# Kernel optimization log

Hardware: AMD Instinct MI355X
Metric: run time of the kernel (lower is better)

## Reference

```python
import jax, jax.numpy as jnp
import numpy as np


def setup_inputs() -> dict:
    key = jax.random.key(0)
    ks = jax.random.split(key, 4)
    B, C, H, W = 8, 256, 64, 64
    C8 = C // 8
    x = jax.random.normal(ks[0], (B, C, H, W), dtype=jnp.float32)
    wq = jax.random.normal(ks[1], (C8, C), dtype=jnp.float32) * 0.05
    wk = jax.random.normal(ks[2], (C8, C), dtype=jnp.float32) * 0.05
    wv = jax.random.normal(ks[3], (C, C), dtype=jnp.float32) * 0.05
    bq = jnp.zeros((C8,), jnp.float32)
    bk = jnp.zeros((C8,), jnp.float32)
    bv = jnp.zeros((C,), jnp.float32)
    return {"x": x, "wq": wq, "bq": bq, "wk": wk, "bk": bk, "wv": wv, "bv": bv}


def _conv1x1(x, w, b):
    # x: [B,C,H,W], w: [O,C], b: [O] -> [B,O,H,W]
    return jnp.einsum('bchw,oc->bohw', x, w) + b[None, :, None, None]


def reference(x, wq, bq, wk, bk, wv, bv):
    B, C, H, W = x.shape
    N = H * W
    q = _conv1x1(x, wq, bq).reshape(B, -1, N)   # [B, C/8, N]
    k = _conv1x1(x, wk, bk).reshape(B, -1, N)   # [B, C/8, N]
    v = _conv1x1(x, wv, bv).reshape(B, C, N)    # [B, C, N]
    # energy[b, n, m] = sum_c q[b, c, n] * k[b, c, m]
    energy = jnp.einsum('bcn,bcm->bnm', q, k)   # [B, N, N]
    attn = jax.nn.softmax(energy, axis=-1)
    # out[b, c, n] = sum_m v[b, c, m] * attn[b, n, m]
    out = jnp.einsum('bcm,bnm->bcn', v, attn)   # [B, C, N]
    return out.reshape(B, C, H, W) + x
```

## Files before the change

### kernel.cpp

```cpp
#include <hip/hip_runtime.h>

#define B_ 8
#define C_ 256
#define C8_ 32
#define N_ 4096

typedef __bf16 bf16;
typedef __bf16 bf16x4 __attribute__((ext_vector_type(4)));
typedef __bf16 bf16x8 __attribute__((ext_vector_type(8)));
typedef float f32x4 __attribute__((ext_vector_type(4)));
typedef float f32x16 __attribute__((ext_vector_type(16)));

#if __has_builtin(__builtin_amdgcn_exp2f)
#define EXP2 __builtin_amdgcn_exp2f
#else
#define EXP2 exp2f
#endif

#define CVTPK(lo, hi) ({ unsigned int _w;                                     \
  asm("v_cvt_pk_bf16_f32 %0, %1, %2" : "=v"(_w) : "v"(lo), "v"(hi)); _w; })
#define LSWAP(a, b) asm("v_permlane32_swap_b32 %0, %1" : "+v"(a), "+v"(b))

#define GLD16(gp, lp) __builtin_amdgcn_global_load_lds(                       \
    (const __attribute__((address_space(1))) void*)(gp),                      \
    (__attribute__((address_space(3))) void*)(lp), 16, 0, 0)
#define VMW(n) do { asm volatile("s_waitcnt vmcnt(" n ")" ::: "memory");      \
    __builtin_amdgcn_sched_barrier(0); } while (0)
#define RBAR() __builtin_amdgcn_s_barrier()

__global__ __launch_bounds__(256) void k_convw(const float* __restrict__ wq,
    const float* __restrict__ wk, const float* __restrict__ wv,
    bf16* __restrict__ Wb) {
  int i = (blockIdx.x * 256 + threadIdx.x) * 4;
  const float* src; int off;
  if (i < 8192) { src = wq; off = i; }
  else if (i < 16384) { src = wk; off = i - 8192; }
  else { src = wv; off = i - 16384; }
  f32x4 v = *reinterpret_cast<const f32x4*>(src + off);
  bf16x4 o;
  o[0] = (bf16)v[0]; o[1] = (bf16)v[1]; o[2] = (bf16)v[2]; o[3] = (bf16)v[3];
  *reinterpret_cast<bf16x4*>(Wb + i) = o;
}

__global__ __launch_bounds__(256) void k_transpose(const float* __restrict__ x,
                                                   bf16* __restrict__ xT) {
  __shared__ bf16 t[64][72];
  int bid = blockIdx.x;
  int b = bid & 7, rem = bid >> 3;
  int c0 = (rem >> 6) * 64, n0 = (rem & 63) * 64;
  int tid = threadIdx.x;
#pragma unroll
  for (int r = 0; r < 4; ++r) {
    int cc = r * 16 + (tid >> 4);
    int j = (tid & 15) * 4;
    f32x4 v = *reinterpret_cast<const f32x4*>(
        x + ((size_t)b * C_ + c0 + cc) * N_ + n0 + j);
    bf16x4 o;
    o[0] = (bf16)v[0]; o[1] = (bf16)v[1]; o[2] = (bf16)v[2]; o[3] = (bf16)v[3];
    *reinterpret_cast<bf16x4*>(&t[cc][j]) = o;
  }
  __syncthreads();
#pragma unroll
  for (int r = 0; r < 2; ++r) {
    int nn = r * 32 + (tid >> 3);
    int c8 = (tid & 7) * 8;
    bf16x8 o;
#pragma unroll
    for (int k = 0; k < 8; ++k) o[k] = t[c8 + k][nn];
    *reinterpret_cast<bf16x8*>(
        xT + ((size_t)b * N_ + n0 + nn) * C_ + c0 + c8) = o;
  }
}

__global__ __launch_bounds__(256) void k_proj_all(const bf16* __restrict__ xT,
    const bf16* __restrict__ Wb, const float* __restrict__ bq,
    const float* __restrict__ bk, const float* __restrict__ bv,
    bf16* __restrict__ Qt, bf16* __restrict__ Kt, bf16* __restrict__ Vt) {
  int bid = blockIdx.x;
  int b = bid & 7, nt = bid >> 3;
  int tid = threadIdx.x, lane = tid & 63, w = tid >> 6;
  int ln = lane & 31, h = lane >> 5;
  int n0 = nt * 128 + w * 32;
  const bf16* xp = xT + ((size_t)b * N_ + n0 + ln) * C_ + h * 8;

  bf16x8 xf[16];
#pragma unroll
  for (int k = 0; k < 16; ++k) xf[k] = *reinterpret_cast<const bf16x8*>(xp + k * 16);

  {
    const bf16* wp = Wb + (size_t)ln * C_ + h * 8;
    bf16x8 wf[16];
#pragma unroll
    for (int k = 0; k < 16; ++k) wf[k] = *reinterpret_cast<const bf16x8*>(wp + k * 16);
    f32x16 acc;
#pragma unroll
    for (int r = 0; r < 16; ++r) acc[r] = 0.f;
#pragma unroll
    for (int k = 0; k < 16; ++k)
      acc = __builtin_amdgcn_mfma_f32_32x32x16_bf16(xf[k], wf[k], acc, 0, 0, 0);
    float bb = bq[ln];
#pragma unroll
    for (int r = 0; r < 16; ++r) {
      int n = n0 + (r & 3) + 8 * (r >> 2) + 4 * h;
      Qt[((size_t)b * N_ + n) * C8_ + ln] = (bf16)((acc[r] + bb) * 1.44269504f);
    }
  }
  {
    const bf16* wp = Wb + 8192 + (size_t)ln * C_ + h * 8;
    bf16x8 wf[16];
#pragma unroll
    for (int k = 0; k < 16; ++k) wf[k] = *reinterpret_cast<const bf16x8*>(wp + k * 16);
    f32x16 acc;
#pragma unroll
    for (int r = 0; r < 16; ++r) acc[r] = 0.f;
#pragma unroll
    for (int k = 0; k < 16; ++k)
      acc = __builtin_amdgcn_mfma_f32_32x32x16_bf16(xf[k], wf[k], acc, 0, 0, 0);
    float bb = bk[ln];
    int f = (ln >> 4) & 1, hA = (ln >> 3) & 1, e = ln & 7;
#pragma unroll
    for (int r = 0; r < 16; ++r) {
      int n = n0 + (r & 3) + 8 * (r >> 2) + 4 * h;
      int mt = n >> 5, lm = n & 31;
      Kt[((size_t)(b * 128 + mt) * 2 + f) * 512 + (lm + hA * 32) * 8 + e] =
          (bf16)(acc[r] + bb);
    }
  }
  int mt = n0 >> 5;
  bf16* tb = Vt + (size_t)(b * 128 + mt) * 8192;
  int j = (ln >> 4) & 1, hA = (ln >> 3) & 1, e = ln & 7;
#pragma unroll 1
  for (int ot = 0; ot < 8; ++ot) {
    const bf16* wp = Wb + 16384 + (size_t)(ot * 32 + ln) * C_ + h * 8;
    bf16x8 wf[16];
#pragma unroll
    for (int k = 0; k < 16; ++k) wf[k] = *reinterpret_cast<const bf16x8*>(wp + k * 16);
    f32x16 acc;
#pragma unroll
    for (int r = 0; r < 16; ++r) acc[r] = 0.f;
#pragma unroll
    for (int k = 0; k < 16; ++k)
      acc = __builtin_amdgcn_mfma_f32_32x32x16_bf16(wf[k], xf[k], acc, 0, 0, 0);
#pragma unroll
    for (int r = 0; r < 16; ++r) {
      int cc = (r & 3) + 8 * (r >> 2) + 4 * h;
      tb[(ot * 2 + j) * 512 + (cc + hA * 32) * 8 + e] =
          (bf16)(acc[r] + bv[ot * 32 + cc]);
    }
  }
}

__global__ __launch_bounds__(256, 2) void k_attn(const bf16* __restrict__ Qt,
    const bf16* __restrict__ Kt, const bf16* __restrict__ Vt,
    const float* __restrict__ x, float* __restrict__ out) {
  __shared__ __align__(16) char sbuf[67584];
  __shared__ float sML[2][2][2][32];
  int bid = blockIdx.x;
  int b = bid & 7;
  int qt = bid >> 3;
  int tid = threadIdx.x, lane = tid & 63, w = tid >> 6;
  int ln = lane & 31, h = lane >> 5;
  int qh = w & 1, mh = w >> 1;
  int n0 = qt * 64 + qh * 32;
  char* bufs = sbuf + mh * 32768;

  const bf16* qp = Qt + ((size_t)b * N_ + n0 + ln) * C8_ + h * 8;
  bf16x8 qf0 = *reinterpret_cast<const bf16x8*>(qp);
  bf16x8 qf1 = *reinterpret_cast<const bf16x8*>(qp + 16);
  const bf16* Kb = Kt + (size_t)(b * 128 + mh * 64) * 1024 + (size_t)lane * 8;
  const char* Vg = (const char*)(Vt + (size_t)(b * 128 + mh * 64) * 8192)
                   + (size_t)lane * 16;

  f32x16 o[8];
#pragma unroll
  for (int ct = 0; ct < 8; ++ct)
#pragma unroll
    for (int r = 0; r < 16; ++r) o[ct][r] = 0.f;
  float M = -1e30f, L = 0.f;

  bf16x8 kf0 = *reinterpret_cast<const bf16x8*>(Kb);
  bf16x8 kf1 = *reinterpret_cast<const bf16x8*>(Kb + 512);
#pragma unroll
  for (int f = 0; f < 8; ++f)
    GLD16(Vg + (qh * 8 + f) * 1024, bufs + (qh * 8 + f) * 1024);
  VMW("8");

  int pp = 0;
#pragma unroll 1
  for (int it = 0; it < 64; ++it) {
    int itn = it + 1 > 63 ? 63 : it + 1;
    bf16x8 kn0 = *reinterpret_cast<const bf16x8*>(Kb + (size_t)itn * 1024);
    bf16x8 kn1 = *reinterpret_cast<const bf16x8*>(Kb + (size_t)itn * 1024 + 512);
    const char* vg = Vg + (size_t)itn * 16384;
    char* bn = bufs + (pp ^ 1) * 16384;
#pragma unroll
    for (int f = 0; f < 8; ++f)
      GLD16(vg + (qh * 8 + f) * 1024, bn + (qh * 8 + f) * 1024);

    f32x16 s;
#pragma unroll
    for (int r = 0; r < 16; ++r) s[r] = 0.f;
    s = __builtin_amdgcn_mfma_f32_32x32x16_bf16(kf0, qf0, s, 0, 0, 0);
    s = __builtin_amdgcn_mfma_f32_32x32x16_bf16(kf1, qf1, s, 0, 0, 0);

    float m0 = fmaxf(fmaxf(fmaxf(s[0], s[1]), fmaxf(s[2], s[3])),
                     fmaxf(fmaxf(s[4], s[5]), fmaxf(s[6], s[7])));
    float m1 = fmaxf(fmaxf(fmaxf(s[8], s[9]), fmaxf(s[10], s[11])),
                     fmaxf(fmaxf(s[12], s[13]), fmaxf(s[14], s[15])));
    float wm = fmaxf(m0, m1);
    wm = fmaxf(wm, __shfl_xor(wm, 32));
    bool resc = __any(wm > M + 8.f);
    if (resc) {
      float Mn = fmaxf(M, wm);
      float sc = EXP2(M - Mn);
      L *= sc;
#pragma unroll
      for (int ct = 0; ct < 8; ++ct)
#pragma unroll
        for (int r = 0; r < 16; ++r) o[ct][r] *= sc;
      M = Mn;
    }
#pragma unroll
    for (int r = 0; r < 16; ++r) s[r] = EXP2(s[r] - M);
    float q0 = (s[0] + s[1]) + (s[2] + s[3]);
    float q1 = (s[4] + s[5]) + (s[6] + s[7]);
    float q2 = (s[8] + s[9]) + (s[10] + s[11]);
    float q3 = (s[12] + s[13]) + (s[14] + s[15]);
    L += (q0 + q1) + (q2 + q3);

    unsigned int c0 = CVTPK(s[0], s[1]),   c1 = CVTPK(s[2], s[3]);
    unsigned int c2 = CVTPK(s[4], s[5]),   c3 = CVTPK(s[6], s[7]);
    unsigned int c4 = CVTPK(s[8], s[9]),   c5 = CVTPK(s[10], s[11]);
    unsigned int c6 = CVTPK(s[12], s[13]), c7 = CVTPK(s[14], s[15]);
    LSWAP(c0, c2); LSWAP(c1, c3); LSWAP(c4, c6); LSWAP(c5, c7);
    union { unsigned int u[4]; bf16x8 v; } P0, P1;
    P0.u[0] = c0; P0.u[1] = c1; P0.u[2] = c2; P0.u[3] = c3;
    P1.u[0] = c4; P1.u[1] = c5; P1.u[2] = c6; P1.u[3] = c7;

    VMW("8");
    RBAR();

    char* bc = bufs + pp * 16384;
    __builtin_amdgcn_s_setprio(1);
#pragma unroll
    for (int ct = 0; ct < 8; ++ct) {
      bf16x8 vf0 = *reinterpret_cast<const bf16x8*>(bc + (2 * ct) * 1024 + lane * 16);
      bf16x8 vf1 = *reinterpret_cast<const bf16x8*>(bc + (2 * ct + 1) * 1024 + lane * 16);
      o[ct] = __builtin_amdgcn_mfma_f32_32x32x16_bf16(vf0, P0.v, o[ct], 0, 0, 0);
      o[ct] = __builtin_amdgcn_mfma_f32_32x32x16_bf16(vf1, P1.v, o[ct], 0, 0, 0);
    }
    __builtin_amdgcn_s_setprio(0);
    RBAR();

    kf0 = kn0; kf1 = kn1;
    pp ^= 1;
  }
  VMW("0");

  L += __shfl_xor(L, 32);
  if (lane < 32) { sML[mh][qh][0][lane] = M; sML[mh][qh][1][lane] = L; }
  __syncthreads();
  float (*Ob)[256][33] = reinterpret_cast<float (*)[256][33]>(sbuf);
  float Ma = sML[0][qh][0][ln], La = sML[0][qh][1][ln];
  float Mb = sML[1][qh][0][ln], Lb = sML[1][qh][1][ln];
  float Ms = fmaxf(Ma, Mb);
  float a0 = EXP2(Ma - Ms), a1 = EXP2(Mb - Ms);
  float inv = 1.f / (La * a0 + Lb * a1);
  float a = mh ? a1 : a0;
  if (mh) {
#pragma unroll
    for (int ct = 0; ct < 8; ++ct)
#pragma unroll
      for (int r = 0; r < 16; ++r) {
        int c = ct * 32 + (r & 3) + 8 * (r >> 2) + 4 * h;
        Ob[qh][c][ln] = o[ct][r] * a;
      }
  }
  __syncthreads();
  if (!mh) {
#pragma unroll
    for (int ct = 0; ct < 8; ++ct)
#pragma unroll
      for (int r = 0; r < 16; ++r) {
        int c = ct * 32 + (r & 3) + 8 * (r >> 2) + 4 * h;
        size_t idx = ((size_t)b * C_ + c) * N_ + n0 + ln;
        out[idx] = (o[ct][r] * a + Ob[qh][c][ln]) * inv + x[idx];
      }
  }
}

extern "C" void kernel_launch(void* const* d_in, const int* in_sizes, int n_in,
                              void* d_out, int out_size, void* d_ws, size_t ws_size,
                              hipStream_t stream) {
  const float* x  = (const float*)d_in[0];
  const float* wq = (const float*)d_in[1];
  const float* bq = (const float*)d_in[2];
  const float* wk = (const float*)d_in[3];
  const float* bk = (const float*)d_in[4];
  const float* wv = (const float*)d_in[5];
  const float* bv = (const float*)d_in[6];
  float* out = (float*)d_out;

  bf16* xT = (bf16*)d_ws;
  bf16* Qt = xT + (size_t)B_ * N_ * C_;
  bf16* Kt = Qt + (size_t)B_ * N_ * C8_;
  bf16* Vt = Kt + (size_t)B_ * N_ * C8_;
  bf16* Wb = Vt + (size_t)B_ * N_ * C_;

  k_convw<<<dim3(80), dim3(256), 0, stream>>>(wq, wk, wv, Wb);
  k_transpose<<<dim3(2048), dim3(256), 0, stream>>>(x, xT);
  k_proj_all<<<dim3(256), dim3(256), 0, stream>>>(xT, Wb, bq, bk, bv, Qt, Kt, Vt);
  k_attn<<<dim3(512), dim3(256), 0, stream>>>(Qt, Kt, Vt, x, out);
}
```

Measured before the change: 151.3 us.

## Software-pipeline softmax one tile ahead of the PV MFMA in attention loop

Restructures the flash-attention main loop so the QK^T scores and exponentials for tile it+1 are computed while the PV MFMAs for tile it consume the previously computed P fragments. K loads are prefetched two tiles ahead, the first tile is peeled into a prologue, and the rescale of the accumulators is deferred until after the PV MFMAs. The aim is to overlap the exp/max VALU work with the matrix cores and to drop one barrier per iteration. In exchange it needs more live registers (extra P fragments and K prefetch) and applies the rescale factor after the accumulation, which changes the order of the arithmetic.

```diff
diff --git a/kernel.cpp b/kernel.cpp
--- a/kernel.cpp
+++ b/kernel.cpp
@@ -176,72 +176,93 @@
   for (int ct = 0; ct < 8; ++ct)
 #pragma unroll
     for (int r = 0; r < 16; ++r) o[ct][r] = 0.f;
-  float M = -1e30f, L = 0.f;
-
-  bf16x8 kf0 = *reinterpret_cast<const bf16x8*>(Kb);
-  bf16x8 kf1 = *reinterpret_cast<const bf16x8*>(Kb + 512);
+  float M, L;
+  union Pu { unsigned int u[4]; bf16x8 v; } P0, P1;
+
+  bf16x8 k00 = *reinterpret_cast<const bf16x8*>(Kb);
+  bf16x8 k01 = *reinterpret_cast<const bf16x8*>(Kb + 512);
 #pragma unroll
   for (int f = 0; f < 8; ++f)
     GLD16(Vg + (qh * 8 + f) * 1024, bufs + (qh * 8 + f) * 1024);
-  VMW("8");
-
-  int pp = 0;
-#pragma unroll 1
-  for (int it = 0; it < 64; ++it) {
-    int itn = it + 1 > 63 ? 63 : it + 1;
-    bf16x8 kn0 = *reinterpret_cast<const bf16x8*>(Kb + (size_t)itn * 1024);
-    bf16x8 kn1 = *reinterpret_cast<const bf16x8*>(Kb + (size_t)itn * 1024 + 512);
-    const char* vg = Vg + (size_t)itn * 16384;
-    char* bn = bufs + (pp ^ 1) * 16384;
-#pragma unroll
-    for (int f = 0; f < 8; ++f)
-      GLD16(vg + (qh * 8 + f) * 1024, bn + (qh * 8 + f) * 1024);
-
+  bf16x8 kf0 = *reinterpret_cast<const bf16x8*>(Kb + 1024);
+  bf16x8 kf1 = *reinterpret_cast<const bf16x8*>(Kb + 1024 + 512);
+  {
     f32x16 s;
 #pragma unroll
     for (int r = 0; r < 16; ++r) s[r] = 0.f;
-    s = __builtin_amdgcn_mfma_f32_32x32x16_bf16(kf0, qf0, s, 0, 0, 0);
-    s = __builtin_amdgcn_mfma_f32_32x32x16_bf16(kf1, qf1, s, 0, 0, 0);
-
+    s = __builtin_amdgcn_mfma_f32_32x32x16_bf16(k00, qf0, s, 0, 0, 0);
+    s = __builtin_amdgcn_mfma_f32_32x32x16_bf16(k01, qf1, s, 0, 0, 0);
     float m0 = fmaxf(fmaxf(fmaxf(s[0], s[1]), fmaxf(s[2], s[3])),
                      fmaxf(fmaxf(s[4], s[5]), fmaxf(s[6], s[7])));
     float m1 = fmaxf(fmaxf(fmaxf(s[8], s[9]), fmaxf(s[10], s[11])),
                      fmaxf(fmaxf(s[12], s[13]), fmaxf(s[14], s[15])));
     float wm = fmaxf(m0, m1);
     wm = fmaxf(wm, __shfl_xor(wm, 32));
-    bool resc = __any(wm > M + 8.f);
-    if (resc) {
-      float Mn = fmaxf(M, wm);
-      float sc = EXP2(M - Mn);
-      L *= sc;
-#pragma unroll
-      for (int ct = 0; ct < 8; ++ct)
-#pragma unroll
-        for (int r = 0; r < 16; ++r) o[ct][r] *= sc;
-      M = Mn;
-    }
+    M = wm;
 #pragma unroll
     for (int r = 0; r < 16; ++r) s[r] = EXP2(s[r] - M);
     float q0 = (s[0] + s[1]) + (s[2] + s[3]);
     float q1 = (s[4] + s[5]) + (s[6] + s[7]);
     float q2 = (s[8] + s[9]) + (s[10] + s[11]);
     float q3 = (s[12] + s[13]) + (s[14] + s[15]);
-    L += (q0 + q1) + (q2 + q3);
-
+    L = (q0 + q1) + (q2 + q3);
     unsigned int c0 = CVTPK(s[0], s[1]),   c1 = CVTPK(s[2], s[3]);
     unsigned int c2 = CVTPK(s[4], s[5]),   c3 = CVTPK(s[6], s[7]);
     unsigned int c4 = CVTPK(s[8], s[9]),   c5 = CVTPK(s[10], s[11]);
     unsigned int c6 = CVTPK(s[12], s[13]), c7 = CVTPK(s[14], s[15]);
     LSWAP(c0, c2); LSWAP(c1, c3); LSWAP(c4, c6); LSWAP(c5, c7);
-    union { unsigned int u[4]; bf16x8 v; } P0, P1;
     P0.u[0] = c0; P0.u[1] = c1; P0.u[2] = c2; P0.u[3] = c3;
     P1.u[0] = c4; P1.u[1] = c5; P1.u[2] = c6; P1.u[3] = c7;
-
-    VMW("8");
-    RBAR();
-
-    char* bc = bufs + pp * 16384;
+  }
+  VMW("2");
+  RBAR();
+
+  int cur = 0;
+#pragma unroll 1
+  for (int it = 0; it < 64; ++it) {
+    int itn = it + 1 > 63 ? 63 : it + 1;
+    int itk = it + 2 > 63 ? 63 : it + 2;
+    char* bc = bufs + cur * 16384;
+    char* bn = bufs + (cur ^ 1) * 16384;
+
+    const char* vg = Vg + (size_t)itn * 16384;
+#pragma unroll
+    for (int f = 0; f < 8; ++f)
+      GLD16(vg + (qh * 8 + f) * 1024, bn + (qh * 8 + f) * 1024);
+
+    f32x16 s;
+#pragma unroll
+    for (int r = 0; r < 16; ++r) s[r] = 0.f;
+    s = __builtin_amdgcn_mfma_f32_32x32x16_bf16(kf0, qf0, s, 0, 0, 0);
+    s = __builtin_amdgcn_mfma_f32_32x32x16_bf16(kf1, qf1, s, 0, 0, 0);
+
+    bf16x8 kn0 = *reinterpret_cast<const bf16x8*>(Kb + (size_t)itk * 1024);
+    bf16x8 kn1 = *reinterpret_cast<const bf16x8*>(Kb + (size_t)itk * 1024 + 512);
+
     __builtin_amdgcn_s_setprio(1);
+    float m0 = fmaxf(fmaxf(fmaxf(s[0], s[1]), fmaxf(s[2], s[3])),
+                     fmaxf(fmaxf(s[4], s[5]), fmaxf(s[6], s[7])));
+    float m1 = fmaxf(fmaxf(fmaxf(s[8], s[9]), fmaxf(s[10], s[11])),
+                     fmaxf(fmaxf(s[12], s[13]), fmaxf(s[14], s[15])));
+    float wm = fmaxf(m0, m1);
+    wm = fmaxf(wm, __shfl_xor(wm, 32));
+    bool commit = it < 63;
+    bool resc = commit && __any(wm > M + 8.f);
+    float Mn = resc ? fmaxf(M, wm) : M;
+    float sc = EXP2(M - Mn);
+#pragma unroll
+    for (int r = 0; r < 16; ++r) s[r] = EXP2(s[r] - Mn);
+    float q0 = (s[0] + s[1]) + (s[2] + s[3]);
+    float q1 = (s[4] + s[5]) + (s[6] + s[7]);
+    float q2 = (s[8] + s[9]) + (s[10] + s[11]);
+    float q3 = (s[12] + s[13]) + (s[14] + s[15]);
+    float ps = (q0 + q1) + (q2 + q3);
+    unsigned int c0 = CVTPK(s[0], s[1]),   c1 = CVTPK(s[2], s[3]);
+    unsigned int c2 = CVTPK(s[4], s[5]),   c3 = CVTPK(s[6], s[7]);
+    unsigned int c4 = CVTPK(s[8], s[9]),   c5 = CVTPK(s[10], s[11]);
+    unsigned int c6 = CVTPK(s[12], s[13]), c7 = CVTPK(s[14], s[15]);
+    LSWAP(c0, c2); LSWAP(c1, c3); LSWAP(c4, c6); LSWAP(c5, c7);
+
 #pragma unroll
     for (int ct = 0; ct < 8; ++ct) {
       bf16x8 vf0 = *reinterpret_cast<const bf16x8*>(bc + (2 * ct) * 1024 + lane * 16);
@@ -250,10 +271,23 @@
       o[ct] = __builtin_amdgcn_mfma_f32_32x32x16_bf16(vf1, P1.v, o[ct], 0, 0, 0);
     }
     __builtin_amdgcn_s_setprio(0);
+
+    if (resc) {
+#pragma unroll
+      for (int ct = 0; ct < 8; ++ct)
+#pragma unroll
+        for (int r = 0; r < 16; ++r) o[ct][r] *= sc;
+    }
+    if (commit) {
+      L = L * sc + ps; M = Mn;
+      P0.u[0] = c0; P0.u[1] = c1; P0.u[2] = c2; P0.u[3] = c3;
+      P1.u[0] = c4; P1.u[1] = c5; P1.u[2] = c6; P1.u[3] = c7;
+    }
+
+    VMW("2");
     RBAR();
-
     kf0 = kn0; kf1 = kn1;
-    pp ^= 1;
+    cur ^= 1;
   }
   VMW("0");
 
```

Result: no change. 152.8 us (+1.0%).

## Fuse transpose into projection kernel, split V projection across grid y, use permlane swap

Applied to the files above, without the earlier changes.

Removes the separate transpose kernel: the projection kernel now reads fp32 x directly, converts it to bf16 and transposes it through shared memory in four channel chunks into MFMA fragments. This avoids writing and re-reading the bf16 xT buffer and drops one launch. The projection grid is doubled along y so one half computes Q, K and the first three V tiles while the other computes the remaining five V tiles. That raises parallelism but means both halves reload and transpose x. Separately, the half-wave max reduction in attention uses v_permlane32_swap instead of a shuffle.

```diff
diff --git a/kernel.cpp b/kernel.cpp
--- a/kernel.cpp
+++ b/kernel.cpp
@@ -20,6 +20,9 @@
 #define CVTPK(lo, hi) ({ unsigned int _w;                                     \
   asm("v_cvt_pk_bf16_f32 %0, %1, %2" : "=v"(_w) : "v"(lo), "v"(hi)); _w; })
 #define LSWAP(a, b) asm("v_permlane32_swap_b32 %0, %1" : "+v"(a), "+v"(b))
+#define HALFMAX(wm) do { float _t;                                            \
+    asm("v_mov_b32 %0, %1" : "=&v"(_t) : "v"(wm));                            \
+    LSWAP(wm, _t); wm = fmaxf(wm, _t); } while (0)
 
 #define GLD16(gp, lp) __builtin_amdgcn_global_load_lds(                       \
     (const __attribute__((address_space(1))) void*)(gp),                      \
@@ -42,53 +45,92 @@
   *reinterpret_cast<bf16x4*>(Wb + i) = o;
 }
 
-__global__ __launch_bounds__(256) void k_transpose(const float* __restrict__ x,
-                                                   bf16* __restrict__ xT) {
-  __shared__ bf16 t[64][72];
-  int bid = blockIdx.x;
-  int b = bid & 7, rem = bid >> 3;
-  int c0 = (rem >> 6) * 64, n0 = (rem & 63) * 64;
-  int tid = threadIdx.x;
-#pragma unroll
-  for (int r = 0; r < 4; ++r) {
-    int cc = r * 16 + (tid >> 4);
-    int j = (tid & 15) * 4;
-    f32x4 v = *reinterpret_cast<const f32x4*>(
-        x + ((size_t)b * C_ + c0 + cc) * N_ + n0 + j);
-    bf16x4 o;
-    o[0] = (bf16)v[0]; o[1] = (bf16)v[1]; o[2] = (bf16)v[2]; o[3] = (bf16)v[3];
-    *reinterpret_cast<bf16x4*>(&t[cc][j]) = o;
-  }
-  __syncthreads();
-#pragma unroll
-  for (int r = 0; r < 2; ++r) {
-    int nn = r * 32 + (tid >> 3);
-    int c8 = (tid & 7) * 8;
-    bf16x8 o;
-#pragma unroll
-    for (int k = 0; k < 8; ++k) o[k] = t[c8 + k][nn];
-    *reinterpret_cast<bf16x8*>(
-        xT + ((size_t)b * N_ + n0 + nn) * C_ + c0 + c8) = o;
-  }
-}
-
-__global__ __launch_bounds__(256) void k_proj_all(const bf16* __restrict__ xT,
+__global__ __launch_bounds__(256) void k_proj_all(const float* __restrict__ x,
     const bf16* __restrict__ Wb, const float* __restrict__ bq,
     const float* __restrict__ bk, const float* __restrict__ bv,
     bf16* __restrict__ Qt, bf16* __restrict__ Kt, bf16* __restrict__ Vt) {
+  __shared__ bf16 sT[64][132];
   int bid = blockIdx.x;
   int b = bid & 7, nt = bid >> 3;
   int tid = threadIdx.x, lane = tid & 63, w = tid >> 6;
   int ln = lane & 31, h = lane >> 5;
-  int n0 = nt * 128 + w * 32;
-  const bf16* xp = xT + ((size_t)b * N_ + n0 + ln) * C_ + h * 8;
+  int n0b = nt * 128;
+  int n0 = n0b + w * 32;
 
   bf16x8 xf[16];
-#pragma unroll
-  for (int k = 0; k < 16; ++k) xf[k] = *reinterpret_cast<const bf16x8*>(xp + k * 16);
-
-  {
-    const bf16* wp = Wb + (size_t)ln * C_ + h * 8;
+#pragma unroll 1
+  for (int ck = 0; ck < 4; ++ck) {
+    int cl = tid >> 5;
+    int j = (tid & 31) * 4;
+#pragma unroll
+    for (int r = 0; r < 8; ++r) {
+      int c = ck * 64 + r * 8 + cl;
+      f32x4 v = *reinterpret_cast<const f32x4*>(
+          x + ((size_t)b * C_ + c) * N_ + n0b + j);
+      bf16x4 o4;
+      o4[0] = (bf16)v[0]; o4[1] = (bf16)v[1]; o4[2] = (bf16)v[2]; o4[3] = (bf16)v[3];
+      *reinterpret_cast<bf16x4*>(&sT[r * 8 + cl][j]) = o4;
+    }
+    __syncthreads();
+#pragma unroll
+    for (int kk = 0; kk < 4; ++kk) {
+      bf16x8 f;
+#pragma unroll
+      for (int e = 0; e < 8; ++e) f[e] = sT[kk * 16 + h * 8 + e][w * 32 + ln];
+      xf[ck * 4 + kk] = f;
+    }
+    __syncthreads();
+  }
+
+  if (blockIdx.y == 0) {
+    {
+      const bf16* wp = Wb + (size_t)ln * C_ + h * 8;
+      bf16x8 wf[16];
+#pragma unroll
+      for (int k = 0; k < 16; ++k) wf[k] = *reinterpret_cast<const bf16x8*>(wp + k * 16);
+      f32x16 acc;
+#pragma unroll
+      for (int r = 0; r < 16; ++r) acc[r] = 0.f;
+#pragma unroll
+      for (int k = 0; k < 16; ++k)
+        acc = __builtin_amdgcn_mfma_f32_32x32x16_bf16(xf[k], wf[k], acc, 0, 0, 0);
+      float bb = bq[ln];
+#pragma unroll
+      for (int r = 0; r < 16; ++r) {
+        int n = n0 + (r & 3) + 8 * (r >> 2) + 4 * h;
+        Qt[((size_t)b * N_ + n) * C8_ + ln] = (bf16)((acc[r] + bb) * 1.44269504f);
+      }
+    }
+    {
+      const bf16* wp = Wb + 8192 + (size_t)ln * C_ + h * 8;
+      bf16x8 wf[16];
+#pragma unroll
+      for (int k = 0; k < 16; ++k) wf[k] = *reinterpret_cast<const bf16x8*>(wp + k * 16);
+      f32x16 acc;
+#pragma unroll
+      for (int r = 0; r < 16; ++r) acc[r] = 0.f;
+#pragma unroll
+      for (int k = 0; k < 16; ++k)
+        acc = __builtin_amdgcn_mfma_f32_32x32x16_bf16(xf[k], wf[k], acc, 0, 0, 0);
+      float bb = bk[ln];
+      int f = (ln >> 4) & 1, hA = (ln >> 3) & 1, e = ln & 7;
+#pragma unroll
+      for (int r = 0; r < 16; ++r) {
+        int n = n0 + (r & 3) + 8 * (r >> 2) + 4 * h;
+        int mt = n >> 5, lm = n & 31;
+        Kt[((size_t)(b * 128 + mt) * 2 + f) * 512 + (lm + hA * 32) * 8 + e] =
+            (bf16)(acc[r] + bb);
+      }
+    }
+  }
+  int mt = n0 >> 5;
+  bf16* tb = Vt + (size_t)(b * 128 + mt) * 8192;
+  int j2 = (ln >> 4) & 1, hA = (ln >> 3) & 1, e = ln & 7;
+  int ot0 = blockIdx.y ? 3 : 0;
+  int ot1 = blockIdx.y ? 8 : 3;
+#pragma unroll 1
+  for (int ot = ot0; ot < ot1; ++ot) {
+    const bf16* wp = Wb + 16384 + (size_t)(ot * 32 + ln) * C_ + h * 8;
     bf16x8 wf[16];
 #pragma unroll
     for (int k = 0; k < 16; ++k) wf[k] = *reinterpret_cast<const bf16x8*>(wp + k * 16);
@@ -97,54 +139,11 @@
     for (int r = 0; r < 16; ++r) acc[r] = 0.f;
 #pragma unroll
     for (int k = 0; k < 16; ++k)
-      acc = __builtin_amdgcn_mfma_f32_32x32x16_bf16(xf[k], wf[k], acc, 0, 0, 0);
-    float bb = bq[ln];
-#pragma unroll
-    for (int r = 0; r < 16; ++r) {
-      int n = n0 + (r & 3) + 8 * (r >> 2) + 4 * h;
-      Qt[((size_t)b * N_ + n) * C8_ + ln] = (bf16)((acc[r] + bb) * 1.44269504f);
-    }
-  }
-  {
-    const bf16* wp = Wb + 8192 + (size_t)ln * C_ + h * 8;
-    bf16x8 wf[16];
-#pragma unroll
-    for (int k = 0; k < 16; ++k) wf[k] = *reinterpret_cast<const bf16x8*>(wp + k * 16);
-    f32x16 acc;
-#pragma unroll
-    for (int r = 0; r < 16; ++r) acc[r] = 0.f;
-#pragma unroll
-    for (int k = 0; k < 16; ++k)
-      acc = __builtin_amdgcn_mfma_f32_32x32x16_bf16(xf[k], wf[k], acc, 0, 0, 0);
-    float bb = bk[ln];
-    int f = (ln >> 4) & 1, hA = (ln >> 3) & 1, e = ln & 7;
-#pragma unroll
-    for (int r = 0; r < 16; ++r) {
-      int n = n0 + (r & 3) + 8 * (r >> 2) + 4 * h;
-      int mt = n >> 5, lm = n & 31;
-      Kt[((size_t)(b * 128 + mt) * 2 + f) * 512 + (lm + hA * 32) * 8 + e] =
-          (bf16)(acc[r] + bb);
-    }
-  }
-  int mt = n0 >> 5;
-  bf16* tb = Vt + (size_t)(b * 128 + mt) * 8192;
-  int j = (ln >> 4) & 1, hA = (ln >> 3) & 1, e = ln & 7;
-#pragma unroll 1
-  for (int ot = 0; ot < 8; ++ot) {
-    const bf16* wp = Wb + 16384 + (size_t)(ot * 32 + ln) * C_ + h * 8;
-    bf16x8 wf[16];
-#pragma unroll
-    for (int k = 0; k < 16; ++k) wf[k] = *reinterpret_cast<const bf16x8*>(wp + k * 16);
-    f32x16 acc;
-#pragma unroll
-    for (int r = 0; r < 16; ++r) acc[r] = 0.f;
-#pragma unroll
-    for (int k = 0; k < 16; ++k)
       acc = __builtin_amdgcn_mfma_f32_32x32x16_bf16(wf[k], xf[k], acc, 0, 0, 0);
 #pragma unroll
     for (int r = 0; r < 16; ++r) {
       int cc = (r & 3) + 8 * (r >> 2) + 4 * h;
-      tb[(ot * 2 + j) * 512 + (cc + hA * 32) * 8 + e] =
+      tb[(ot * 2 + j2) * 512 + (cc + hA * 32) * 8 + e] =
           (bf16)(acc[r] + bv[ot * 32 + cc]);
     }
   }
@@ -208,7 +207,7 @@
     float m1 = fmaxf(fmaxf(fmaxf(s[8], s[9]), fmaxf(s[10], s[11])),
                      fmaxf(fmaxf(s[12], s[13]), fmaxf(s[14], s[15])));
     float wm = fmaxf(m0, m1);
-    wm = fmaxf(wm, __shfl_xor(wm, 32));
+    HALFMAX(wm);
     bool resc = __any(wm > M + 8.f);
     if (resc) {
       float Mn = fmaxf(M, wm);
@@ -301,14 +300,12 @@
   const float* bv = (const float*)d_in[6];
   float* out = (float*)d_out;
 
-  bf16* xT = (bf16*)d_ws;
-  bf16* Qt = xT + (size_t)B_ * N_ * C_;
+  bf16* Qt = (bf16*)d_ws;
   bf16* Kt = Qt + (size_t)B_ * N_ * C8_;
   bf16* Vt = Kt + (size_t)B_ * N_ * C8_;
   bf16* Wb = Vt + (size_t)B_ * N_ * C_;
 
   k_convw<<<dim3(80), dim3(256), 0, stream>>>(wq, wk, wv, Wb);
-  k_transpose<<<dim3(2048), dim3(256), 0, stream>>>(x, xT);
-  k_proj_all<<<dim3(256), dim3(256), 0, stream>>>(xT, Wb, bq, bk, bv, Qt, Kt, Vt);
+  k_proj_all<<<dim3(256, 2), dim3(256), 0, stream>>>(x, Wb, bq, bk, bv, Qt, Kt, Vt);
   k_attn<<<dim3(512), dim3(256), 0, stream>>>(Qt, Kt, Vt, x, out);
 }
```

After: 152.0 us. About the same (+0.4%).

## Fuse weight conversion into transpose, split projection work across more blocks

Applied to the files above, without the earlier changes.

The weight bf16 conversion is folded into the first 80 blocks of the transpose kernel, which removes one launch. The projection kernel now launches 512 blocks of 64 positions each instead of 256 blocks of 128. Within each block, the waves split the Q/K and V output tiles between them (3 and 5 V tiles) to get better CU occupancy. In attention, the cross-half max reduction uses v_permlane32_swap instead of a shuffle, which avoids LDS-based ds_bpermute. The trade-off is that each x fragment is reloaded by two waves, and the per-wave work is imbalanced.

```diff
diff --git a/kernel.cpp b/kernel.cpp
--- a/kernel.cpp
+++ b/kernel.cpp
@@ -20,6 +20,9 @@
 #define CVTPK(lo, hi) ({ unsigned int _w;                                     \
   asm("v_cvt_pk_bf16_f32 %0, %1, %2" : "=v"(_w) : "v"(lo), "v"(hi)); _w; })
 #define LSWAP(a, b) asm("v_permlane32_swap_b32 %0, %1" : "+v"(a), "+v"(b))
+#define HALFMAX(wm) do { float _t;                                            \
+    asm("v_mov_b32 %0, %1" : "=&v"(_t) : "v"(wm));                            \
+    LSWAP(wm, _t); wm = fmaxf(wm, _t); } while (0)
 
 #define GLD16(gp, lp) __builtin_amdgcn_global_load_lds(                       \
     (const __attribute__((address_space(1))) void*)(gp),                      \
@@ -28,27 +31,26 @@
     __builtin_amdgcn_sched_barrier(0); } while (0)
 #define RBAR() __builtin_amdgcn_s_barrier()
 
-__global__ __launch_bounds__(256) void k_convw(const float* __restrict__ wq,
+__global__ __launch_bounds__(256) void k_transpose(const float* __restrict__ x,
+    bf16* __restrict__ xT, const float* __restrict__ wq,
     const float* __restrict__ wk, const float* __restrict__ wv,
     bf16* __restrict__ Wb) {
-  int i = (blockIdx.x * 256 + threadIdx.x) * 4;
-  const float* src; int off;
-  if (i < 8192) { src = wq; off = i; }
-  else if (i < 16384) { src = wk; off = i - 8192; }
-  else { src = wv; off = i - 16384; }
-  f32x4 v = *reinterpret_cast<const f32x4*>(src + off);
-  bf16x4 o;
-  o[0] = (bf16)v[0]; o[1] = (bf16)v[1]; o[2] = (bf16)v[2]; o[3] = (bf16)v[3];
-  *reinterpret_cast<bf16x4*>(Wb + i) = o;
-}
-
-__global__ __launch_bounds__(256) void k_transpose(const float* __restrict__ x,
-                                                   bf16* __restrict__ xT) {
   __shared__ bf16 t[64][72];
   int bid = blockIdx.x;
+  int tid = threadIdx.x;
+  if (bid < 80) {
+    int i = (bid * 256 + tid) * 4;
+    const float* src; int off;
+    if (i < 8192) { src = wq; off = i; }
+    else if (i < 16384) { src = wk; off = i - 8192; }
+    else { src = wv; off = i - 16384; }
+    f32x4 v = *reinterpret_cast<const f32x4*>(src + off);
+    bf16x4 o;
+    o[0] = (bf16)v[0]; o[1] = (bf16)v[1]; o[2] = (bf16)v[2]; o[3] = (bf16)v[3];
+    *reinterpret_cast<bf16x4*>(Wb + i) = o;
+  }
   int b = bid & 7, rem = bid >> 3;
   int c0 = (rem >> 6) * 64, n0 = (rem & 63) * 64;
-  int tid = threadIdx.x;
 #pragma unroll
   for (int r = 0; r < 4; ++r) {
     int cc = r * 16 + (tid >> 4);
@@ -72,7 +74,7 @@
   }
 }
 
-__global__ __launch_bounds__(256) void k_proj_all(const bf16* __restrict__ xT,
+__global__ __launch_bounds__(256) void k_proj(const bf16* __restrict__ xT,
     const bf16* __restrict__ Wb, const float* __restrict__ bq,
     const float* __restrict__ bk, const float* __restrict__ bv,
     bf16* __restrict__ Qt, bf16* __restrict__ Kt, bf16* __restrict__ Vt) {
@@ -80,15 +82,63 @@
   int b = bid & 7, nt = bid >> 3;
   int tid = threadIdx.x, lane = tid & 63, w = tid >> 6;
   int ln = lane & 31, h = lane >> 5;
-  int n0 = nt * 128 + w * 32;
+  int nsub = w & 1, og = w >> 1;
+  int n0 = nt * 64 + nsub * 32;
   const bf16* xp = xT + ((size_t)b * N_ + n0 + ln) * C_ + h * 8;
 
   bf16x8 xf[16];
 #pragma unroll
   for (int k = 0; k < 16; ++k) xf[k] = *reinterpret_cast<const bf16x8*>(xp + k * 16);
 
-  {
-    const bf16* wp = Wb + (size_t)ln * C_ + h * 8;
+  if (og == 0) {
+    {
+      const bf16* wp = Wb + (size_t)ln * C_ + h * 8;
+      bf16x8 wf[16];
+#pragma unroll
+      for (int k = 0; k < 16; ++k) wf[k] = *reinterpret_cast<const bf16x8*>(wp + k * 16);
+      f32x16 acc;
+#pragma unroll
+      for (int r = 0; r < 16; ++r) acc[r] = 0.f;
+#pragma unroll
+      for (int k = 0; k < 16; ++k)
+        acc = __builtin_amdgcn_mfma_f32_32x32x16_bf16(xf[k], wf[k], acc, 0, 0, 0);
+      float bb = bq[ln];
+#pragma unroll
+      for (int r = 0; r < 16; ++r) {
+        int n = n0 + (r & 3) + 8 * (r >> 2) + 4 * h;
+        Qt[((size_t)b * N_ + n) * C8_ + ln] = (bf16)((acc[r] + bb) * 1.44269504f);
+      }
+    }
+    {
+      const bf16* wp = Wb + 8192 + (size_t)ln * C_ + h * 8;
+      bf16x8 wf[16];
+#pragma unroll
+      for (int k = 0; k < 16; ++k) wf[k] = *reinterpret_cast<const bf16x8*>(wp + k * 16);
+      f32x16 acc;
+#pragma unroll
+      for (int r = 0; r < 16; ++r) acc[r] = 0.f;
+#pragma unroll
+      for (int k = 0; k < 16; ++k)
+        acc = __builtin_amdgcn_mfma_f32_32x32x16_bf16(xf[k], wf[k], acc, 0, 0, 0);
+      float bb = bk[ln];
+      int f = (ln >> 4) & 1, hA = (ln >> 3) & 1, e = ln & 7;
+#pragma unroll
+      for (int r = 0; r < 16; ++r) {
+        int n = n0 + (r & 3) + 8 * (r >> 2) + 4 * h;
+        int mt = n >> 5, lm = n & 31;
+        Kt[((size_t)(b * 128 + mt) * 2 + f) * 512 + (lm + hA * 32) * 8 + e] =
+            (bf16)(acc[r] + bb);
+      }
+    }
+  }
+  int mt = n0 >> 5;
+  bf16* tb = Vt + (size_t)(b * 128 + mt) * 8192;
+  int j2 = (ln >> 4) & 1, hA = (ln >> 3) & 1, e = ln & 7;
+  int ot0 = og ? 3 : 0;
+  int ot1 = og ? 8 : 3;
+#pragma unroll 1
+  for (int ot = ot0; ot < ot1; ++ot) {
+    const bf16* wp = Wb + 16384 + (size_t)(ot * 32 + ln) * C_ + h * 8;
     bf16x8 wf[16];
 #pragma unroll
     for (int k = 0; k < 16; ++k) wf[k] = *reinterpret_cast<const bf16x8*>(wp + k * 16);
@@ -97,54 +147,11 @@
     for (int r = 0; r < 16; ++r) acc[r] = 0.f;
 #pragma unroll
     for (int k = 0; k < 16; ++k)
-      acc = __builtin_amdgcn_mfma_f32_32x32x16_bf16(xf[k], wf[k], acc, 0, 0, 0);
-    float bb = bq[ln];
-#pragma unroll
-    for (int r = 0; r < 16; ++r) {
-      int n = n0 + (r & 3) + 8 * (r >> 2) + 4 * h;
-      Qt[((size_t)b * N_ + n) * C8_ + ln] = (bf16)((acc[r] + bb) * 1.44269504f);
-    }
-  }
-  {
-    const bf16* wp = Wb + 8192 + (size_t)ln * C_ + h * 8;
-    bf16x8 wf[16];
-#pragma unroll
-    for (int k = 0; k < 16; ++k) wf[k] = *reinterpret_cast<const bf16x8*>(wp + k * 16);
-    f32x16 acc;
-#pragma unroll
-    for (int r = 0; r < 16; ++r) acc[r] = 0.f;
-#pragma unroll
-    for (int k = 0; k < 16; ++k)
-      acc = __builtin_amdgcn_mfma_f32_32x32x16_bf16(xf[k], wf[k], acc, 0, 0, 0);
-    float bb = bk[ln];
-    int f = (ln >> 4) & 1, hA = (ln >> 3) & 1, e = ln & 7;
-#pragma unroll
-    for (int r = 0; r < 16; ++r) {
-      int n = n0 + (r & 3) + 8 * (r >> 2) + 4 * h;
-      int mt = n >> 5, lm = n & 31;
-      Kt[((size_t)(b * 128 + mt) * 2 + f) * 512 + (lm + hA * 32) * 8 + e] =
-          (bf16)(acc[r] + bb);
-    }
-  }
-  int mt = n0 >> 5;
-  bf16* tb = Vt + (size_t)(b * 128 + mt) * 8192;
-  int j = (ln >> 4) & 1, hA = (ln >> 3) & 1, e = ln & 7;
-#pragma unroll 1
-  for (int ot = 0; ot < 8; ++ot) {
-    const bf16* wp = Wb + 16384 + (size_t)(ot * 32 + ln) * C_ + h * 8;
-    bf16x8 wf[16];
-#pragma unroll
-    for (int k = 0; k < 16; ++k) wf[k] = *reinterpret_cast<const bf16x8*>(wp + k * 16);
-    f32x16 acc;
-#pragma unroll
-    for (int r = 0; r < 16; ++r) acc[r] = 0.f;
-#pragma unroll
-    for (int k = 0; k < 16; ++k)
       acc = __builtin_amdgcn_mfma_f32_32x32x16_bf16(wf[k], xf[k], acc, 0, 0, 0);
 #pragma unroll
     for (int r = 0; r < 16; ++r) {
       int cc = (r & 3) + 8 * (r >> 2) + 4 * h;
-      tb[(ot * 2 + j) * 512 + (cc + hA * 32) * 8 + e] =
+      tb[(ot * 2 + j2) * 512 + (cc + hA * 32) * 8 + e] =
           (bf16)(acc[r] + bv[ot * 32 + cc]);
     }
   }
@@ -208,7 +215,7 @@
     float m1 = fmaxf(fmaxf(fmaxf(s[8], s[9]), fmaxf(s[10], s[11])),
                      fmaxf(fmaxf(s[12], s[13]), fmaxf(s[14], s[15])));
     float wm = fmaxf(m0, m1);
-    wm = fmaxf(wm, __shfl_xor(wm, 32));
+    HALFMAX(wm);
     bool resc = __any(wm > M + 8.f);
     if (resc) {
       float Mn = fmaxf(M, wm);
@@ -307,8 +314,7 @@
   bf16* Vt = Kt + (size_t)B_ * N_ * C8_;
   bf16* Wb = Vt + (size_t)B_ * N_ * C_;
 
-  k_convw<<<dim3(80), dim3(256), 0, stream>>>(wq, wk, wv, Wb);
-  k_transpose<<<dim3(2048), dim3(256), 0, stream>>>(x, xT);
-  k_proj_all<<<dim3(256), dim3(256), 0, stream>>>(xT, Wb, bq, bk, bv, Qt, Kt, Vt);
+  k_transpose<<<dim3(2048), dim3(256), 0, stream>>>(x, xT, wq, wk, wv, Wb);
+  k_proj<<<dim3(512), dim3(256), 0, stream>>>(xT, Wb, bq, bk, bv, Qt, Kt, Vt);
   k_attn<<<dim3(512), dim3(256), 0, stream>>>(Qt, Kt, Vt, x, out);
 }
```

New measurement: 143.6 us. -5.1%, faster.
